# Kernel optimization log

Measured on AMD Instinct MI355X. Metric: run time of the kernel, lower is better.

The kernel has to match this reference:

```python
import jax, jax.numpy as jnp
import numpy as np

B, N, D, K = 512, 262144, 512, 10


def setup_inputs() -> dict:
    key = jax.random.key(0)
    k1, k2 = jax.random.split(key)
    image_embs = jax.random.normal(k1, (B, D), dtype=jnp.float32)
    index = jax.random.normal(k2, (N, D), dtype=jnp.float32)  # baked-in text embeddings
    return {"image_embs": image_embs, "index": index, "k": K}


def reference(image_embs, index, k):
    # sims: [B, N] inner-product similarities (IndexFlatIP)
    sims = image_embs @ index.T
    _, idx = jax.lax.top_k(sims, k)  # sorted descending, matches torch.topk
    return idx.astype(jnp.int32)
```

## Files before the change

### kernel.cpp

```cpp
#include <hip/hip_runtime.h>
#include <stdint.h>

#define B_Q   512
#define N_IDX 262144
#define D_DIM 512
#define TOPK  10
#define CAND  6

constexpr int BM = 256, BN = 64, BK = 32;
constexpr int CHUNKS = 256;
constexpr int NR = N_IDX / CHUNKS;
constexpr int NT = NR / BN;
constexpr int KT = D_DIM / BK;
constexpr int ITERS = NT * KT;
constexpr int NCAND = CHUNKS * CAND;

typedef _Float16 half8  __attribute__((ext_vector_type(8)));
typedef float    f32x4  __attribute__((ext_vector_type(4)));

__device__ __forceinline__ unsigned int pk16(float a, float b)
{
    return __builtin_bit_cast(unsigned int, __builtin_amdgcn_cvt_pkrtz(a, b));
}

__device__ __forceinline__ void glds16(const void* g, char* lds)
{
    __builtin_amdgcn_global_load_lds(
        (const __attribute__((address_space(1))) void*)g,
        (__attribute__((address_space(3))) void*)lds, 16, 0, 0);
}

__global__ __launch_bounds__(256)
void qprep(const float* __restrict__ Q, _Float16* __restrict__ Qsw)
{
    const int n = blockIdx.x * 256 + threadIdx.x;
    const float4 p0 = reinterpret_cast<const float4*>(Q)[n * 2];
    const float4 p1 = reinterpret_cast<const float4*>(Q)[n * 2 + 1];
    uint4 u;
    u.x = pk16(p0.x, p0.y);
    u.y = pk16(p0.z, p0.w);
    u.z = pk16(p1.x, p1.y);
    u.w = pk16(p1.z, p1.w);
    const int kslot = n & 63, rowg = n >> 6;
    const int kt = kslot >> 2, slot = kslot & 3;
    const int qt = rowg >> 8, row = rowg & 255;
    reinterpret_cast<uint4*>(Qsw)[(qt * 16 + kt) * 1024 + slot * 256 + row] = u;
}

__global__ __launch_bounds__(512, 4)
void faiss_p1(const _Float16* __restrict__ Qsw, const float* __restrict__ X,
              float* __restrict__ cand_v, int* __restrict__ cand_i)
{
    __shared__ __align__(16) char smem[57344];
    float* Cs = (float*)(smem + 40960);

    const int tid  = threadIdx.x;
    const int lane = tid & 63;
    const int w    = tid >> 6;
    const int wm   = w >> 1;
    const int wn   = w & 1;
    const int bc   = blockIdx.x >> 1;
    const int qt   = blockIdx.x & 1;
    const int row0 = qt * 256;

    const _Float16* Aglob = Qsw + (size_t)qt * 131072;
    const int aG0 = w * 128 + lane, aG1 = aG0 + 64;
    const int aD0 = w * 2048, aD1 = aD0 + 1024;

    const int brow = tid >> 3, bq = tid & 7;
    const float* Xb = X + (size_t)(bc * NR + brow) * D_DIM + bq * 4;
    const int bD = ((bq >> 1) * 64 + brow) * 16 + (bq & 1) * 8;

    int a_off[4], b_off[2];
#pragma unroll
    for (int mi = 0; mi < 4; ++mi)
        a_off[mi] = ((lane >> 4) * 256 + wm * 64 + mi * 16 + (lane & 15)) * 16;
#pragma unroll
    for (int ni = 0; ni < 2; ++ni)
        b_off[ni] = ((lane >> 4) * 64 + wn * 32 + ni * 16 + (lane & 15)) * 16;

    float topv[CAND]; int topi[CAND];
#pragma unroll
    for (int j = 0; j < CAND; ++j) { topv[j] = -3.0e38f; topi[j] = 0; }

    f32x4 acc[4][2];
#pragma unroll
    for (int mi = 0; mi < 4; ++mi) { acc[mi][0] = (f32x4)0.0f; acc[mi][1] = (f32x4)0.0f; }

    float4 bE, bO;
    glds16(Aglob + (size_t)aG0 * 8, smem + aD0);
    glds16(Aglob + (size_t)aG1 * 8, smem + aD1);
    __builtin_amdgcn_sched_barrier(0);
    bE = *(const float4*)(Xb);
    bO = *(const float4*)(Xb + 32);
    __builtin_amdgcn_sched_barrier(0);

    auto step = [&](int j, float4& bset) {
        if (j == 0 || j == ITERS - 1)
            asm volatile("s_waitcnt vmcnt(0)" ::: "memory");
        else
            asm volatile("s_waitcnt vmcnt(1)" ::: "memory");
        {
            uint2 u;
            u.x = pk16(bset.x, bset.y);
            u.y = pk16(bset.z, bset.w);
            *(uint2*)(smem + 32768 + (j & 1) * 4096 + bD) = u;
        }
        asm volatile("s_waitcnt lgkmcnt(0)" ::: "memory");
        __builtin_amdgcn_s_barrier();
        if (j + 1 < ITERS) {
            const int kn = ((j + 1) & 15) * 1024;
            char* dst = smem + ((j + 1) & 1) * 16384;
            glds16(Aglob + (size_t)(kn + aG0) * 8, dst + aD0);
            glds16(Aglob + (size_t)(kn + aG1) * 8, dst + aD1);
        }
        __builtin_amdgcn_sched_barrier(0);
        if (j + 2 < ITERS) {
            const int j2 = j + 2;
            bset = *(const float4*)(Xb + (size_t)(j2 >> 4) * (BN * D_DIM) + (j2 & 15) * 32);
        }
        __builtin_amdgcn_sched_barrier(0);
        const char* Ab = smem + (j & 1) * 16384;
        const char* Bb = smem + 32768 + (j & 1) * 4096;
        half8 af[4];
#pragma unroll
        for (int mi = 0; mi < 4; ++mi)
            af[mi] = *(const half8*)(Ab + a_off[mi]);
        const half8 bf0 = *(const half8*)(Bb + b_off[0]);
        const half8 bf1 = *(const half8*)(Bb + b_off[1]);
#pragma unroll
        for (int mi = 0; mi < 4; ++mi) {
            acc[mi][0] = __builtin_amdgcn_mfma_f32_16x16x32_f16(af[mi], bf0, acc[mi][0], 0, 0, 0);
            acc[mi][1] = __builtin_amdgcn_mfma_f32_16x16x32_f16(af[mi], bf1, acc[mi][1], 0, 0, 0);
        }
        if ((j & 15) == 15) {
            const int colbase = bc * NR + (j >> 4) * BN;
#pragma unroll
            for (int s = 0; s < 4; ++s) {
                if (wn == (s >> 1)) {
                    const int ni = s & 1;
#pragma unroll
                    for (int mi = 0; mi < 4; ++mi)
#pragma unroll
                        for (int r = 0; r < 4; ++r) {
                            const int rr = wm * 64 + mi * 16 + (lane >> 4) * 4 + r;
                            Cs[rr * 16 + ((lane & 15) ^ ((rr >> 1) & 15))] = acc[mi][ni][r];
                        }
                }
                asm volatile("s_waitcnt lgkmcnt(0)" ::: "memory");
                __builtin_amdgcn_s_barrier();
                if (tid < 256) {
                    const int r = tid;
                    const int base = colbase + s * 16;
                    for (int c = 0; c < 16; ++c) {
                        const float v = Cs[r * 16 + (c ^ ((r >> 1) & 15))];
                        const int id = base + c;
                        if (v > topv[CAND - 1] ||
                            (v == topv[CAND - 1] && id < topi[CAND - 1])) {
                            topv[CAND - 1] = v; topi[CAND - 1] = id;
#pragma unroll
                            for (int t = CAND - 1; t > 0; --t) {
                                const bool gt = topv[t] > topv[t - 1] ||
                                    (topv[t] == topv[t - 1] && topi[t] < topi[t - 1]);
                                if (gt) {
                                    const float tv = topv[t]; topv[t] = topv[t - 1]; topv[t - 1] = tv;
                                    const int   ti = topi[t]; topi[t] = topi[t - 1]; topi[t - 1] = ti;
                                }
                            }
                        }
                    }
                }
                asm volatile("s_waitcnt lgkmcnt(0)" ::: "memory");
                __builtin_amdgcn_s_barrier();
            }
#pragma unroll
            for (int mi = 0; mi < 4; ++mi) { acc[mi][0] = (f32x4)0.0f; acc[mi][1] = (f32x4)0.0f; }
        }
    };

    for (int jj = 0; jj < ITERS; jj += 2) {
        step(jj,     bE);
        step(jj + 1, bO);
    }

    if (tid < 256) {
        const size_t base = ((size_t)(row0 + tid) * CHUNKS + bc) * CAND;
#pragma unroll
        for (int j = 0; j < CAND; ++j) {
            cand_v[base + j] = topv[j];
            cand_i[base + j] = topi[j];
        }
    }
}

__global__ __launch_bounds__(256)
void faiss_p2(const float* __restrict__ cand_v, const int* __restrict__ cand_i,
              const float* __restrict__ Q, const float* __restrict__ X,
              int* __restrict__ out)
{
    __shared__ float vs[NCAND];
    __shared__ int   is[NCAND];
    __shared__ float qs[D_DIM];
    __shared__ int   Sidx[NCAND];
    __shared__ float Sval[NCAND];
    __shared__ int   scount;
    __shared__ float pivV;
    __shared__ int   pivI;

    const int row = blockIdx.x, tid = threadIdx.x;

    for (int i = tid; i < NCAND; i += 256) {
        vs[i] = cand_v[(size_t)row * NCAND + i];
        is[i] = cand_i[(size_t)row * NCAND + i];
    }
    if (tid < 128)
        ((float4*)qs)[tid] = ((const float4*)(Q + (size_t)row * D_DIM))[tid];
    if (tid == 0) scount = 0;
    __syncthreads();

    {
        const float h = vs[tid * CAND];
        const int  hid = is[tid * CAND];
        int r = 0;
        for (int j = 0; j < CHUNKS; ++j) {
            const float vj = vs[j * CAND];
            r += (vj > h) || (vj == h && is[j * CAND] < hid);
        }
        if (r == 23) { pivV = h; pivI = hid; }
    }
    __syncthreads();

    const float pv = pivV; const int pi = pivI;
    for (int i = tid; i < NCAND; i += 256) {
        const float v = vs[i]; const int id = is[i];
        if (v > pv || (v == pv && id <= pi)) {
            const int p = atomicAdd(&scount, 1);
            Sidx[p] = id;
        }
    }
    __syncthreads();
    const int nS = scount;

    const int wv = tid >> 6, ln = tid & 63;
    for (int si = wv; si < nS; si += 4) {
        const float* xr = X + (size_t)Sidx[si] * D_DIM + ln * 8;
        const float4 xa = *(const float4*)(xr);
        const float4 xb = *(const float4*)(xr + 4);
        const float* qp = qs + ln * 8;
        float s = 0.0f;
        s = fmaf(qp[0], xa.x, s); s = fmaf(qp[1], xa.y, s);
        s = fmaf(qp[2], xa.z, s); s = fmaf(qp[3], xa.w, s);
        s = fmaf(qp[4], xb.x, s); s = fmaf(qp[5], xb.y, s);
        s = fmaf(qp[6], xb.z, s); s = fmaf(qp[7], xb.w, s);
#pragma unroll
        for (int off = 32; off > 0; off >>= 1)
            s += __shfl_down(s, off);
        if (ln == 0) Sval[si] = s;
    }
    __syncthreads();

    for (int i = tid; i < nS; i += 256) {
        const float v = Sval[i]; const int id = Sidx[i];
        int r = 0;
        for (int j = 0; j < nS; ++j) {
            const float vj = Sval[j];
            r += (vj > v) || (vj == v && Sidx[j] < id);
        }
        if (r < TOPK) out[row * TOPK + r] = id;
    }
}

extern "C" void kernel_launch(void* const* d_in, const int* in_sizes, int n_in,
                              void* d_out, int out_size, void* d_ws, size_t ws_size,
                              hipStream_t stream)
{
    (void)in_sizes; (void)n_in; (void)out_size; (void)ws_size;
    const float* Q = (const float*)d_in[0];
    const float* X = (const float*)d_in[1];
    int* out = (int*)d_out;

    char* ws = (char*)d_ws;
    float*    cand_v = (float*)ws;
    int*      cand_i = (int*)(ws + (size_t)B_Q * NCAND * 4);
    _Float16* Qsw    = (_Float16*)(ws + (size_t)B_Q * NCAND * 8);

    qprep<<<dim3(B_Q * D_DIM / 8 / 256), dim3(256), 0, stream>>>(Q, Qsw);
    faiss_p1<<<dim3(512), dim3(512), 0, stream>>>(Qsw, X, cand_v, cand_i);
    faiss_p2<<<dim3(B_Q), dim3(256), 0, stream>>>(cand_v, cand_i, Q, X, out);
}
```

Before: 510.1 us.

## Enlarge GEMM tile to 128x64 per step with 4x4 MFMA accumulators per wave

Doubles the N tile and the K depth per iteration, so each wave now holds 4x4 accumulators and issues 32 MFMAs per barrier instead of 8. The aim is to amortise barriers and LDS traffic over more work. The query pre-swizzle layout and the X load pattern change to match the new tiling. The epilogue now uses a padded stride-34 C tile and processes 32 columns per pass. Shared memory grows to about 130 KB and occupancy falls to 2 blocks per CU, which could hurt latency hiding.

```diff
diff --git a/kernel.cpp b/kernel.cpp
--- a/kernel.cpp
+++ b/kernel.cpp
@@ -7,16 +7,17 @@
 #define TOPK  10
 #define CAND  6
 
-constexpr int BM = 256, BN = 64, BK = 32;
+constexpr int BM = 256, BN = 128, BK = 64;
 constexpr int CHUNKS = 256;
 constexpr int NR = N_IDX / CHUNKS;
 constexpr int NT = NR / BN;
 constexpr int KT = D_DIM / BK;
 constexpr int ITERS = NT * KT;
 constexpr int NCAND = CHUNKS * CAND;
-
-typedef _Float16 half8  __attribute__((ext_vector_type(8)));
-typedef float    f32x4  __attribute__((ext_vector_type(4)));
+constexpr int CS_STRIDE = 34;
+
+typedef _Float16 half8 __attribute__((ext_vector_type(8)));
+typedef float    f32x4 __attribute__((ext_vector_type(4)));
 
 __device__ __forceinline__ unsigned int pk16(float a, float b)
 {
@@ -31,129 +32,159 @@
 }
 
 __global__ __launch_bounds__(256)
-void qprep(const float* __restrict__ Q, _Float16* __restrict__ Qsw)
+void qprep(const float* __restrict__ Q, uint4* __restrict__ QswU4)
 {
     const int n = blockIdx.x * 256 + threadIdx.x;
-    const float4 p0 = reinterpret_cast<const float4*>(Q)[n * 2];
-    const float4 p1 = reinterpret_cast<const float4*>(Q)[n * 2 + 1];
+    const int qt = n >> 14, row = (n >> 6) & 255, kt = (n >> 3) & 7, ks = n & 7;
+    const float4* src = reinterpret_cast<const float4*>(Q)
+                        + ((qt * 256 + row) * 128 + kt * 16 + ks * 2);
+    const float4 p0 = src[0], p1 = src[1];
     uint4 u;
     u.x = pk16(p0.x, p0.y);
     u.y = pk16(p0.z, p0.w);
     u.z = pk16(p1.x, p1.y);
     u.w = pk16(p1.z, p1.w);
-    const int kslot = n & 63, rowg = n >> 6;
-    const int kt = kslot >> 2, slot = kslot & 3;
-    const int qt = rowg >> 8, row = rowg & 255;
-    reinterpret_cast<uint4*>(Qsw)[(qt * 16 + kt) * 1024 + slot * 256 + row] = u;
-}
-
-__global__ __launch_bounds__(512, 4)
-void faiss_p1(const _Float16* __restrict__ Qsw, const float* __restrict__ X,
+    QswU4[(qt * 8 + kt) * 2048 + ks * 256 + row] = u;
+}
+
+__global__ __launch_bounds__(512, 2)
+void faiss_p1(const uint4* __restrict__ QswU4, const float* __restrict__ X,
               float* __restrict__ cand_v, int* __restrict__ cand_i)
 {
-    __shared__ __align__(16) char smem[57344];
-    float* Cs = (float*)(smem + 40960);
+    __shared__ __align__(16) char smem[133120];
+    float* Cs = (float*)(smem + 98304);
 
     const int tid  = threadIdx.x;
     const int lane = tid & 63;
     const int w    = tid >> 6;
     const int wm   = w >> 1;
     const int wn   = w & 1;
-    const int bc   = blockIdx.x >> 1;
-    const int qt   = blockIdx.x & 1;
-    const int row0 = qt * 256;
-
-    const _Float16* Aglob = Qsw + (size_t)qt * 131072;
-    const int aG0 = w * 128 + lane, aG1 = aG0 + 64;
-    const int aD0 = w * 2048, aD1 = aD0 + 1024;
-
-    const int brow = tid >> 3, bq = tid & 7;
-    const float* Xb = X + (size_t)(bc * NR + brow) * D_DIM + bq * 4;
-    const int bD = ((bq >> 1) * 64 + brow) * 16 + (bq & 1) * 8;
-
-    int a_off[4], b_off[2];
+    const int chunk = blockIdx.x >> 1;
+    const int qt    = blockIdx.x & 1;
+    const int row0  = qt * 256;
+
+    const uint4* Abase = QswU4 + (size_t)qt * 8 * 2048;
+
+    const int bcol = tid >> 2, bkq = tid & 3;
+    const float* Xbase = X + (size_t)(chunk * NR + bcol) * D_DIM + bkq * 16;
+    const int bD0 = ((bkq * 2) * 128 + bcol) * 16;
+    const int bD1 = bD0 + 128 * 16;
+
+    int a_off[2][4], b_off[2][4];
+#pragma unroll
+    for (int kk = 0; kk < 2; ++kk) {
+#pragma unroll
+        for (int mi = 0; mi < 4; ++mi)
+            a_off[kk][mi] = ((kk * 4 + (lane >> 4)) * 256 + wm * 64 + mi * 16 + (lane & 15)) * 16;
+#pragma unroll
+        for (int ni = 0; ni < 4; ++ni)
+            b_off[kk][ni] = ((kk * 4 + (lane >> 4)) * 128 + wn * 64 + ni * 16 + (lane & 15)) * 16;
+    }
+
+    float topv[CAND]; int topi[CAND];
+#pragma unroll
+    for (int j = 0; j < CAND; ++j) { topv[j] = -3.0e38f; topi[j] = 0; }
+
+    f32x4 acc[4][4];
 #pragma unroll
     for (int mi = 0; mi < 4; ++mi)
-        a_off[mi] = ((lane >> 4) * 256 + wm * 64 + mi * 16 + (lane & 15)) * 16;
-#pragma unroll
-    for (int ni = 0; ni < 2; ++ni)
-        b_off[ni] = ((lane >> 4) * 64 + wn * 32 + ni * 16 + (lane & 15)) * 16;
-
-    float topv[CAND]; int topi[CAND];
-#pragma unroll
-    for (int j = 0; j < CAND; ++j) { topv[j] = -3.0e38f; topi[j] = 0; }
-
-    f32x4 acc[4][2];
-#pragma unroll
-    for (int mi = 0; mi < 4; ++mi) { acc[mi][0] = (f32x4)0.0f; acc[mi][1] = (f32x4)0.0f; }
-
-    float4 bE, bO;
-    glds16(Aglob + (size_t)aG0 * 8, smem + aD0);
-    glds16(Aglob + (size_t)aG1 * 8, smem + aD1);
+#pragma unroll
+        for (int ni = 0; ni < 4; ++ni) acc[mi][ni] = (f32x4)0.0f;
+
+    float4 breg[4];
+
+    auto issueB = [&](int j) {
+        const int nt2 = j >> 3, kt2 = j & 7;
+        const float* p = Xbase + (size_t)nt2 * (BN * D_DIM) + kt2 * 64;
+#pragma unroll
+        for (int q = 0; q < 4; ++q)
+            breg[q] = *reinterpret_cast<const float4*>(p + q * 4);
+    };
+    auto issueA = [&](int j) {
+        const uint4* src = Abase + (j & 7) * 2048;
+        char* dst = smem + (j & 1) * 32768;
+#pragma unroll
+        for (int i = 0; i < 4; ++i)
+            glds16(src + w * 256 + i * 64 + lane, dst + (w * 256 + i * 64) * 16);
+    };
+    auto writeB = [&](int j) {
+        char* bb = smem + 65536 + (j & 1) * 16384;
+        uint4 u0, u1;
+        u0.x = pk16(breg[0].x, breg[0].y); u0.y = pk16(breg[0].z, breg[0].w);
+        u0.z = pk16(breg[1].x, breg[1].y); u0.w = pk16(breg[1].z, breg[1].w);
+        u1.x = pk16(breg[2].x, breg[2].y); u1.y = pk16(breg[2].z, breg[2].w);
+        u1.z = pk16(breg[3].x, breg[3].y); u1.w = pk16(breg[3].z, breg[3].w);
+        *(uint4*)(bb + bD0) = u0;
+        *(uint4*)(bb + bD1) = u1;
+    };
+
+    issueB(0);
     __builtin_amdgcn_sched_barrier(0);
-    bE = *(const float4*)(Xb);
-    bO = *(const float4*)(Xb + 32);
+    issueA(0);
     __builtin_amdgcn_sched_barrier(0);
-
-    auto step = [&](int j, float4& bset) {
-        if (j == 0 || j == ITERS - 1)
-            asm volatile("s_waitcnt vmcnt(0)" ::: "memory");
-        else
-            asm volatile("s_waitcnt vmcnt(1)" ::: "memory");
+    asm volatile("s_waitcnt vmcnt(4)" ::: "memory");
+    writeB(0);
+    asm volatile("s_waitcnt vmcnt(0)" ::: "memory");
+    __syncthreads();
+
+    for (int j = 0; j < ITERS; ++j) {
+        if (j + 1 < ITERS) {
+            issueB(j + 1);
+            __builtin_amdgcn_sched_barrier(0);
+            issueA(j + 1);
+        }
+        __builtin_amdgcn_sched_barrier(0);
+
         {
-            uint2 u;
-            u.x = pk16(bset.x, bset.y);
-            u.y = pk16(bset.z, bset.w);
-            *(uint2*)(smem + 32768 + (j & 1) * 4096 + bD) = u;
-        }
-        asm volatile("s_waitcnt lgkmcnt(0)" ::: "memory");
-        __builtin_amdgcn_s_barrier();
+            const char* ab = smem + (j & 1) * 32768;
+            const char* bb = smem + 65536 + (j & 1) * 16384;
+#pragma unroll
+            for (int kk = 0; kk < 2; ++kk) {
+                half8 af[4], bf[4];
+#pragma unroll
+                for (int mi = 0; mi < 4; ++mi)
+                    af[mi] = *reinterpret_cast<const half8*>(ab + a_off[kk][mi]);
+#pragma unroll
+                for (int ni = 0; ni < 4; ++ni)
+                    bf[ni] = *reinterpret_cast<const half8*>(bb + b_off[kk][ni]);
+#pragma unroll
+                for (int mi = 0; mi < 4; ++mi)
+#pragma unroll
+                    for (int ni = 0; ni < 4; ++ni)
+                        acc[mi][ni] = __builtin_amdgcn_mfma_f32_16x16x32_f16(
+                            af[mi], bf[ni], acc[mi][ni], 0, 0, 0);
+            }
+        }
+        __builtin_amdgcn_sched_barrier(0);
+
         if (j + 1 < ITERS) {
-            const int kn = ((j + 1) & 15) * 1024;
-            char* dst = smem + ((j + 1) & 1) * 16384;
-            glds16(Aglob + (size_t)(kn + aG0) * 8, dst + aD0);
-            glds16(Aglob + (size_t)(kn + aG1) * 8, dst + aD1);
-        }
-        __builtin_amdgcn_sched_barrier(0);
-        if (j + 2 < ITERS) {
-            const int j2 = j + 2;
-            bset = *(const float4*)(Xb + (size_t)(j2 >> 4) * (BN * D_DIM) + (j2 & 15) * 32);
-        }
-        __builtin_amdgcn_sched_barrier(0);
-        const char* Ab = smem + (j & 1) * 16384;
-        const char* Bb = smem + 32768 + (j & 1) * 4096;
-        half8 af[4];
-#pragma unroll
-        for (int mi = 0; mi < 4; ++mi)
-            af[mi] = *(const half8*)(Ab + a_off[mi]);
-        const half8 bf0 = *(const half8*)(Bb + b_off[0]);
-        const half8 bf1 = *(const half8*)(Bb + b_off[1]);
-#pragma unroll
-        for (int mi = 0; mi < 4; ++mi) {
-            acc[mi][0] = __builtin_amdgcn_mfma_f32_16x16x32_f16(af[mi], bf0, acc[mi][0], 0, 0, 0);
-            acc[mi][1] = __builtin_amdgcn_mfma_f32_16x16x32_f16(af[mi], bf1, acc[mi][1], 0, 0, 0);
-        }
-        if ((j & 15) == 15) {
-            const int colbase = bc * NR + (j >> 4) * BN;
+            asm volatile("s_waitcnt vmcnt(4)" ::: "memory");
+            writeB(j + 1);
+        }
+        __syncthreads();
+
+        if ((j & 7) == 7) {
+            const int col0g = chunk * NR + (j >> 3) * BN;
 #pragma unroll
             for (int s = 0; s < 4; ++s) {
                 if (wn == (s >> 1)) {
-                    const int ni = s & 1;
-#pragma unroll
-                    for (int mi = 0; mi < 4; ++mi)
-#pragma unroll
-                        for (int r = 0; r < 4; ++r) {
-                            const int rr = wm * 64 + mi * 16 + (lane >> 4) * 4 + r;
-                            Cs[rr * 16 + ((lane & 15) ^ ((rr >> 1) & 15))] = acc[mi][ni][r];
-                        }
+                    const int nbase = (s & 1) * 2;
+#pragma unroll
+                    for (int nn = 0; nn < 2; ++nn)
+#pragma unroll
+                        for (int mi = 0; mi < 4; ++mi)
+#pragma unroll
+                            for (int r = 0; r < 4; ++r) {
+                                const int row = wm * 64 + mi * 16 + (lane >> 4) * 4 + r;
+                                const int cc  = nn * 16 + (lane & 15);
+                                Cs[row * CS_STRIDE + cc] = acc[mi][nbase + nn][r];
+                            }
                 }
-                asm volatile("s_waitcnt lgkmcnt(0)" ::: "memory");
-                __builtin_amdgcn_s_barrier();
+                __syncthreads();
                 if (tid < 256) {
-                    const int r = tid;
-                    const int base = colbase + s * 16;
-                    for (int c = 0; c < 16; ++c) {
-                        const float v = Cs[r * 16 + (c ^ ((r >> 1) & 15))];
+                    const int base = col0g + s * 32;
+                    for (int c = 0; c < 32; ++c) {
+                        const float v = Cs[tid * CS_STRIDE + c];
                         const int id = base + c;
                         if (v > topv[CAND - 1] ||
                             (v == topv[CAND - 1] && id < topi[CAND - 1])) {
@@ -170,21 +201,17 @@
                         }
                     }
                 }
-                asm volatile("s_waitcnt lgkmcnt(0)" ::: "memory");
-                __builtin_amdgcn_s_barrier();
+                __syncthreads();
             }
 #pragma unroll
-            for (int mi = 0; mi < 4; ++mi) { acc[mi][0] = (f32x4)0.0f; acc[mi][1] = (f32x4)0.0f; }
-        }
-    };
-
-    for (int jj = 0; jj < ITERS; jj += 2) {
-        step(jj,     bE);
-        step(jj + 1, bO);
+            for (int mi = 0; mi < 4; ++mi)
+#pragma unroll
+                for (int ni = 0; ni < 4; ++ni) acc[mi][ni] = (f32x4)0.0f;
+        }
     }
 
     if (tid < 256) {
-        const size_t base = ((size_t)(row0 + tid) * CHUNKS + bc) * CAND;
+        const size_t base = ((size_t)(row0 + tid) * CHUNKS + chunk) * CAND;
 #pragma unroll
         for (int j = 0; j < CAND; ++j) {
             cand_v[base + j] = topv[j];
@@ -280,11 +307,11 @@
     int* out = (int*)d_out;
 
     char* ws = (char*)d_ws;
-    float*    cand_v = (float*)ws;
-    int*      cand_i = (int*)(ws + (size_t)B_Q * NCAND * 4);
-    _Float16* Qsw    = (_Float16*)(ws + (size_t)B_Q * NCAND * 8);
-
-    qprep<<<dim3(B_Q * D_DIM / 8 / 256), dim3(256), 0, stream>>>(Q, Qsw);
-    faiss_p1<<<dim3(512), dim3(512), 0, stream>>>(Qsw, X, cand_v, cand_i);
+    float* cand_v = (float*)ws;
+    int*   cand_i = (int*)(ws + (size_t)B_Q * NCAND * 4);
+    uint4* QswU4  = (uint4*)(ws + (size_t)B_Q * NCAND * 8);
+
+    qprep<<<dim3(128), dim3(256), 0, stream>>>(Q, QswU4);
+    faiss_p1<<<dim3(512), dim3(512), 0, stream>>>(QswU4, X, cand_v, cand_i);
     faiss_p2<<<dim3(B_Q), dim3(256), 0, stream>>>(cand_v, cand_i, Q, X, out);
 }
```

New measurement: 969.1 us. +90.0%, slower.
